# Optimization experiments

Hardware: AMD Instinct MI355X
Metric: run time of the kernel (lower is better)

## Reference

```python
import jax, jax.numpy as jnp
import numpy as np

N_ROI = 400
N_GRAPHS = 256
N = N_ROI * N_GRAPHS        # 102400 total nodes (stacked graphs)
E = N * 32                  # 3276800 edges, avg degree 32
T = 64                      # n_timepoints (in_channels of conv1)
H = 32                      # hidden channels of conv1/conv2
BS = 16                     # batch_size init arg = out_channels of conv3
N_CLASSES = 9


def setup_inputs() -> dict:
    key = jax.random.key(0)
    ks = jax.random.split(key, 20)
    s = 0.05
    p = {
        "x": jax.random.normal(ks[0], (N, T), jnp.float32),
        "edge_index": jax.random.randint(ks[1], (2, E), 0, N, dtype=jnp.int32),
        "edge_weight": jax.random.uniform(ks[2], (E,), jnp.float32),
        # ChebConv K=2: two bias-free linears + shared bias per layer
        "W1_0": jax.random.normal(ks[3], (T, H), jnp.float32) * s,
        "W1_1": jax.random.normal(ks[4], (T, H), jnp.float32) * s,
        "b1": jnp.zeros((H,), jnp.float32),
        "W2_0": jax.random.normal(ks[5], (H, H), jnp.float32) * s,
        "W2_1": jax.random.normal(ks[6], (H, H), jnp.float32) * s,
        "b2": jnp.zeros((H,), jnp.float32),
        "W3_0": jax.random.normal(ks[7], (H, BS), jnp.float32) * s,
        "W3_1": jax.random.normal(ks[8], (H, BS), jnp.float32) * s,
        "b3": jnp.zeros((BS,), jnp.float32),
        "fc1_w": jax.random.normal(ks[9], (N_ROI * BS, 256), jnp.float32) * s,
        "fc1_b": jnp.zeros((256,), jnp.float32),
        "fc2_w": jax.random.normal(ks[10], (256, 128), jnp.float32) * s,
        "fc2_b": jnp.zeros((128,), jnp.float32),
        "fc3_w": jax.random.normal(ks[11], (128, N_CLASSES), jnp.float32) * s,
        "fc3_b": jnp.zeros((N_CLASSES,), jnp.float32),
    }
    return p


def reference(x, edge_index, edge_weight, W1_0, W1_1, b1, W2_0, W2_1, b2,
              W3_0, W3_1, b3, fc1_w, fc1_b, fc2_w, fc2_b, fc3_w, fc3_b):
    src, dst = edge_index[0], edge_index[1]
    n = x.shape[0]
    # sym-normalized scaled Laplacian (lambda_max=2): Lhat = -D^-1/2 A D^-1/2
    deg = jax.ops.segment_sum(edge_weight, src, num_segments=n)
    deg_safe = jnp.where(deg > 0, deg, 1.0)
    dinv = jnp.where(deg > 0, jax.lax.rsqrt(deg_safe), 0.0)
    lapw = -(dinv[src] * edge_weight * dinv[dst])  # [E]

    def cheb(h, W0, W1, b):
        # K=2: Tx0 = h, Tx1 = Lhat @ h (gather-scatter over edges)
        tx1 = jax.ops.segment_sum(lapw[:, None] * h[src], dst, num_segments=n)
        return h @ W0 + tx1 @ W1 + b

    h = jax.nn.relu(cheb(x, W1_0, W1_1, b1))     # [N, 32]
    h = jax.nn.relu(cheb(h, W2_0, W2_1, b2))     # [N, 32]
    h = jax.nn.relu(cheb(h, W3_0, W3_1, b3))     # [N, 16]
    # global_mean_pool with batch=arange(N) is identity; reshape to graphs
    h = h.reshape(-1, N_ROI * BS)                # [256, 6400]
    h = h @ fc1_w + fc1_b                        # dropout is eval-mode identity
    h = h @ fc2_w + fc2_b
    return h @ fc3_w + fc3_b                     # [256, 9]
```

## Files before the change

### kernel.cpp

```cpp
#include <hip/hip_runtime.h>

#define NN   102400
#define NE   3276800
#define TT   64
#define HH   32
#define BSC  16
#define NG   256
#define NC   9
#define F1   256
#define F2   128
#define FIN  6400

#define NBUCK 200
#define CAP   18432
#define TILE  8192


__global__ __launch_bounds__(256) void k_init(int* __restrict__ scur,
                                              int* __restrict__ dcur) {
    int t = threadIdx.x;
    if (t < NBUCK) { scur[t] = t * CAP; dcur[t] = t * CAP; }
}

template<int MODE>
__global__ __launch_bounds__(256) void k_part(const int* __restrict__ src,
                                              const int* __restrict__ dst,
                                              const float* __restrict__ ew,
                                              int* __restrict__ gcur,
                                              int2* __restrict__ outbuf) {
    __shared__ int hist[256];
    __shared__ int base[256];
    __shared__ int cur[256];
    __shared__ int gpos[256];
    __shared__ int2 stage[TILE];
    __shared__ unsigned char bkt[TILE];

    int t = threadIdx.x;
    int e0 = blockIdx.x * TILE;

    hist[t] = 0;
    __syncthreads();
#pragma unroll
    for (int i = 0; i < TILE / 256; ++i) {
        int e = e0 + i * 256 + t;
        int key = MODE ? dst[e] : src[e];
        atomicAdd(&hist[key >> 9], 1);
    }
    __syncthreads();
    int h = hist[t];
    base[t] = h;
    __syncthreads();
    for (int off = 1; off < 256; off <<= 1) {
        int add = (t >= off) ? base[t - off] : 0;
        __syncthreads();
        base[t] += add;
        __syncthreads();
    }
    int excl = base[t] - h;
    __syncthreads();
    base[t] = excl;
    cur[t] = excl;
    __syncthreads();
#pragma unroll
    for (int i = 0; i < TILE / 256; ++i) {
        int e = e0 + i * 256 + t;
        int s = src[e];
        int w = __float_as_int(ew[e]);
        int key, pack;
        if (MODE) { int d = dst[e]; key = d; pack = (s << 9) | (d & 511); }
        else      { key = s; pack = s & 511; }
        int b = key >> 9;
        int p = atomicAdd(&cur[b], 1);
        stage[p] = make_int2(pack, w);
        bkt[p] = (unsigned char)b;
    }
    __syncthreads();
    if (t < NBUCK && h > 0) gpos[t] = atomicAdd(&gcur[t], h);
    __syncthreads();
#pragma unroll
    for (int i = 0; i < TILE / 256; ++i) {
        int p = i * 256 + t;
        int b = bkt[p];
        outbuf[gpos[b] + (p - base[b])] = stage[p];
    }
}


__global__ __launch_bounds__(512) void k_deg2(const int* __restrict__ scur,
                                              const int2* __restrict__ sbuck,
                                              float* __restrict__ dinv) {
    __shared__ float acc[512];
    int b = blockIdx.x, t = threadIdx.x;
    acc[t] = 0.f;
    __syncthreads();
    int lo = b * CAP, hi = scur[b];
    for (int j = lo + t; j < hi; j += 512) {
        int2 e = sbuck[j];
        atomicAdd(&acc[e.x], __int_as_float(e.y));
    }
    __syncthreads();
    float v = acc[t];
    dinv[b * 512 + t] = v > 0.f ? rsqrtf(v) : 0.f;
}


__global__ __launch_bounds__(512) void k_fin(const int* __restrict__ dcur,
                                             const int2* __restrict__ dbuck,
                                             const float* __restrict__ dinv,
                                             int2* __restrict__ edata,
                                             int* __restrict__ rowbeg,
                                             int* __restrict__ rowend) {
    __shared__ float dl[512];
    __shared__ int cnt[512];
    __shared__ int base[512];
    __shared__ int cur[512];
    int b = blockIdx.x, t = threadIdx.x;
    dl[t] = dinv[b * 512 + t];
    cnt[t] = 0;
    __syncthreads();
    int lo = b * CAP, hi = dcur[b];
    for (int j = lo + t; j < hi; j += 512)
        atomicAdd(&cnt[dbuck[j].x & 511], 1);
    __syncthreads();
    int h = cnt[t];
    base[t] = h;
    __syncthreads();
    for (int off = 1; off < 512; off <<= 1) {
        int add = (t >= off) ? base[t - off] : 0;
        __syncthreads();
        base[t] += add;
        __syncthreads();
    }
    int beg = lo + base[t] - h;
    rowbeg[b * 512 + t] = beg;
    rowend[b * 512 + t] = beg + h;
    cur[t] = beg;
    __syncthreads();
    for (int j = lo + t; j < hi; j += 512) {
        int2 e = dbuck[j];
        int dlow = e.x & 511;
        int s = e.x >> 9;
        float lw = -dinv[s] * __int_as_float(e.y) * dl[dlow];
        int slot = atomicAdd(&cur[dlow], 1);
        edata[slot] = make_int2(s, __float_as_int(lw));
    }
}


__global__ __launch_bounds__(256) void k_sortrows(const int* __restrict__ rowbeg,
                                                  const int* __restrict__ rowend,
                                                  int2* __restrict__ edata) {
    int wave = threadIdx.x >> 6;
    int lane = threadIdx.x & 63;
    int node = blockIdx.x * 4 + wave;
    int beg = rowbeg[node], end = rowend[node];
    int len = end - beg;
    if (len > 64 || len <= 1) return;
    unsigned long long key;
    if (lane < len) {
        int2 e = edata[beg + lane];
        key = ((unsigned long long)(unsigned)e.x << 32) | (unsigned)e.y;
    } else {
        key = ~0ULL;
    }
#pragma unroll
    for (int k = 2; k <= 64; k <<= 1) {
#pragma unroll
        for (int j = k >> 1; j >= 1; j >>= 1) {
            unsigned long long other = __shfl_xor(key, j, 64);
            bool lower = (lane & j) == 0;
            bool asc   = (lane & k) == 0;
            unsigned long long mn = key < other ? key : other;
            unsigned long long mx = key < other ? other : key;
            key = (lower == asc) ? mn : mx;
        }
    }
    if (lane < len) {
        edata[beg + lane] = make_int2((int)(key >> 32),
                                      (int)(unsigned)(key & 0xFFFFFFFFu));
    }
}

template<int CIN, int COUT>
__global__ __launch_bounds__(256) void k_dual_gemm(const float* __restrict__ in,
                                                   const float* __restrict__ W0,
                                                   const float* __restrict__ W1,
                                                   float* __restrict__ o0,
                                                   float* __restrict__ o1) {
    int node = blockIdx.x * 256 + threadIdx.x;
    const float* row = in + (size_t)node * CIN;
    float a0[COUT], a1[COUT];
#pragma unroll
    for (int c = 0; c < COUT; ++c) { a0[c] = 0.f; a1[c] = 0.f; }
    for (int k = 0; k < CIN; ++k) {
        float xv = row[k];
#pragma unroll
        for (int c = 0; c < COUT; ++c) {
            a0[c] = fmaf(xv, W0[k * COUT + c], a0[c]);
            a1[c] = fmaf(xv, W1[k * COUT + c], a1[c]);
        }
    }
#pragma unroll
    for (int c = 0; c < COUT; ++c) {
        o0[(size_t)node * COUT + c] = a0[c];
        o1[(size_t)node * COUT + c] = a1[c];
    }
}

template<int C>
__global__ __launch_bounds__(256) void k_gather(const int* __restrict__ rowbeg,
                                                const int* __restrict__ rowend,
                                                const int2* __restrict__ edata,
                                                const float* __restrict__ xw,
                                                const float* __restrict__ a,
                                                const float* __restrict__ bias,
                                                float* __restrict__ out) {
    constexpr int L = C / 2;
    constexpr int NPB = 256 / L;
    int tid = threadIdx.x;
    int g = tid / L;
    int lane = tid % L;
    int node = blockIdx.x * NPB + g;
    int start = rowbeg[node], end = rowend[node];
    const float2* xw2 = (const float2*)xw;
    float accx = 0.f, accy = 0.f;
    int j = start;
    for (; j + 7 < end; j += 8) {
        int2 e[8];
        float2 v[8];
#pragma unroll
        for (int u = 0; u < 8; ++u) e[u] = edata[j + u];
#pragma unroll
        for (int u = 0; u < 8; ++u) v[u] = xw2[(size_t)e[u].x * L + lane];
#pragma unroll
        for (int u = 0; u < 8; ++u) {
            float w = __int_as_float(e[u].y);
            accx = fmaf(w, v[u].x, accx);
            accy = fmaf(w, v[u].y, accy);
        }
    }
    for (; j < end; ++j) {
        int2 e0 = edata[j];
        float2 v0 = xw2[(size_t)e0.x * L + lane];
        float w = __int_as_float(e0.y);
        accx = fmaf(w, v0.x, accx);
        accy = fmaf(w, v0.y, accy);
    }
    float2 av = ((const float2*)a)[(size_t)node * L + lane];
    float2 bv = ((const float2*)bias)[lane];
    float rx = av.x + accx + bv.x;
    float ry = av.y + accy + bv.y;
    float2 r;
    r.x = rx > 0.f ? rx : 0.f;
    r.y = ry > 0.f ? ry : 0.f;
    ((float2*)out)[(size_t)node * L + lane] = r;
}

__global__ __launch_bounds__(256) void k_w23(const float* __restrict__ fc2w,
                                             const float* __restrict__ fc3w,
                                             float* __restrict__ w23) {
    int gid = blockIdx.x * 256 + threadIdx.x;
    if (gid >= F1 * NC) return;
    int r = gid / NC, c = gid % NC;
    float acc = 0.f;
    for (int j = 0; j < F2; ++j) acc = fmaf(fc2w[r * F2 + j], fc3w[j * NC + c], acc);
    w23[gid] = acc;
}

__global__ __launch_bounds__(64) void k_bc(const float* __restrict__ fc1b,
                                           const float* __restrict__ fc2b,
                                           const float* __restrict__ fc3b,
                                           const float* __restrict__ fc3w,
                                           const float* __restrict__ w23,
                                           float* __restrict__ bc) {
    int c = threadIdx.x;
    if (c >= NC) return;
    float acc = fc3b[c];
    for (int k = 0; k < F1; ++k) acc = fmaf(fc1b[k], w23[k * NC + c], acc);
    for (int j = 0; j < F2; ++j) acc = fmaf(fc2b[j], fc3w[j * NC + c], acc);
    bc[c] = acc;
}

__global__ __launch_bounds__(256) void k_t1(const float* __restrict__ fc1w,
                                            const float* __restrict__ fc2w,
                                            float* __restrict__ t1) {
    int c = threadIdx.x & 127;
    int rh = threadIdx.x >> 7;
    int r0 = blockIdx.x * 16 + rh;
    float acc[8];
#pragma unroll
    for (int rr = 0; rr < 8; ++rr) acc[rr] = 0.f;
    for (int k = 0; k < F1; ++k) {
        float wv = fc2w[k * F2 + c];
#pragma unroll
        for (int rr = 0; rr < 8; ++rr)
            acc[rr] = fmaf(fc1w[(r0 + rr * 2) * F1 + k], wv, acc[rr]);
    }
#pragma unroll
    for (int rr = 0; rr < 8; ++rr) t1[(r0 + rr * 2) * F2 + c] = acc[rr];
}

__global__ __launch_bounds__(256) void k_wc(const float* __restrict__ t1,
                                            const float* __restrict__ fc3w,
                                            float* __restrict__ wc) {
    int gid = blockIdx.x * 256 + threadIdx.x;
    int r = gid >> 4, c = gid & 15;
    if (c >= NC) return;
    float acc = 0.f;
    for (int j = 0; j < F2; ++j) acc = fmaf(t1[r * F2 + j], fc3w[j * NC + c], acc);
    wc[r * NC + c] = acc;
}

__global__ __launch_bounds__(256) void k_out(const float* __restrict__ h3,
                                             const float* __restrict__ wc,
                                             const float* __restrict__ bc,
                                             float* __restrict__ out) {
    __shared__ float red[256 * 10];
    int g = blockIdx.x, tid = threadIdx.x;
    float acc[NC];
#pragma unroll
    for (int c = 0; c < NC; ++c) acc[c] = 0.f;
    for (int k = tid; k < FIN; k += 256) {
        float hv = h3[(size_t)g * FIN + k];
#pragma unroll
        for (int c = 0; c < NC; ++c) acc[c] = fmaf(hv, wc[k * NC + c], acc[c]);
    }
#pragma unroll
    for (int c = 0; c < NC; ++c) red[tid * 10 + c] = acc[c];
    __syncthreads();
    for (int s = 128; s > 0; s >>= 1) {
        if (tid < s) {
#pragma unroll
            for (int c = 0; c < NC; ++c) red[tid * 10 + c] += red[(tid + s) * 10 + c];
        }
        __syncthreads();
    }
    if (tid < NC) out[g * NC + tid] = red[tid] + bc[tid];
}


extern "C" void kernel_launch(void* const* d_in, const int* in_sizes, int n_in,
                              void* d_out, int out_size, void* d_ws, size_t ws_size,
                              hipStream_t stream) {
    const float* x    = (const float*)d_in[0];
    const int*   ei   = (const int*)d_in[1];
    const float* ew   = (const float*)d_in[2];
    const float* W1_0 = (const float*)d_in[3];
    const float* W1_1 = (const float*)d_in[4];
    const float* b1   = (const float*)d_in[5];
    const float* W2_0 = (const float*)d_in[6];
    const float* W2_1 = (const float*)d_in[7];
    const float* b2   = (const float*)d_in[8];
    const float* W3_0 = (const float*)d_in[9];
    const float* W3_1 = (const float*)d_in[10];
    const float* b3   = (const float*)d_in[11];
    const float* fc1w = (const float*)d_in[12];
    const float* fc1b = (const float*)d_in[13];
    const float* fc2w = (const float*)d_in[14];
    const float* fc2b = (const float*)d_in[15];
    const float* fc3w = (const float*)d_in[16];
    const float* fc3b = (const float*)d_in[17];
    float* out = (float*)d_out;
    float* ws  = (float*)d_ws;

    const int* src = ei;
    const int* dst = ei + NE;

    const size_t REG = (size_t)NBUCK * CAP;
    float* dinv  = ws;
    int2*  dbuck = (int2*)(dinv + NN);
    int2*  sbuck = dbuck + REG;
    int2*  edata = sbuck;
    float* D     = (float*)(sbuck + REG);
    int*   rowbeg = (int*)(D + (size_t)NN * HH);
    int*   rowend = rowbeg + NN;
    int*   scur   = rowend + NN;
    int*   dcur   = scur + ((NBUCK + 1) & ~1);
    float* w23    = (float*)(dcur + ((NBUCK + 1) & ~1));
    float* bc     = w23 + F1 * NC;

    float* A = (float*)dbuck;
    float* B = A + (size_t)NN * HH;

    k_init<<<1, 256, 0, stream>>>(scur, dcur);
    k_part<0><<<NE / TILE, 256, 0, stream>>>(src, dst, ew, scur, sbuck);
    k_part<1><<<NE / TILE, 256, 0, stream>>>(src, dst, ew, dcur, dbuck);
    k_deg2<<<NBUCK, 512, 0, stream>>>(scur, sbuck, dinv);
    k_fin<<<NBUCK, 512, 0, stream>>>(dcur, dbuck, dinv, edata, rowbeg, rowend);
    k_sortrows<<<NN / 4, 256, 0, stream>>>(rowbeg, rowend, edata);

    k_dual_gemm<TT, HH><<<NN / 256, 256, 0, stream>>>(x, W1_0, W1_1, A, B);
    k_gather<HH><<<NN / 16, 256, 0, stream>>>(rowbeg, rowend, edata, B, A, b1, D);

    k_dual_gemm<HH, HH><<<NN / 256, 256, 0, stream>>>(D, W2_0, W2_1, A, B);
    k_gather<HH><<<NN / 16, 256, 0, stream>>>(rowbeg, rowend, edata, B, A, b2, D);

    k_dual_gemm<HH, BSC><<<NN / 256, 256, 0, stream>>>(D, W3_0, W3_1, A, B);
    k_gather<BSC><<<NN / 32, 256, 0, stream>>>(rowbeg, rowend, edata, B, A, b3, D);

    k_w23<<<(F1 * NC + 255) / 256, 256, 0, stream>>>(fc2w, fc3w, w23);
    k_bc<<<1, 64, 0, stream>>>(fc1b, fc2b, fc3b, fc3w, w23, bc);
    float* T1 = A;
    k_t1<<<FIN / 16, 256, 0, stream>>>(fc1w, fc2w, T1);
    float* Wc = B;
    k_wc<<<FIN * 16 / 256, 256, 0, stream>>>(T1, fc3w, Wc);
    k_out<<<NG, 256, 0, stream>>>(D, Wc, bc, out);
}
```

Measured before the change: 632.5 us.

## Fuse layer-2 gather with layer-3 dual GEMM and drop per-row edge sort

Removes the bitonic per-row sort of edge data and fuses the second Chebyshev gather with the third layer's dual linear transform via intra-group shuffles. This avoids writing and re-reading a 32-channel intermediate, one kernel launch, and the sort pass. Buffers are remapped so the later layer and head outputs fit in the freed regions. Unsorted rows make summation order nondeterministic and may reduce gather locality.

```diff
diff --git a/kernel.cpp b/kernel.cpp
--- a/kernel.cpp
+++ b/kernel.cpp
@@ -143,41 +143,6 @@
         float lw = -dinv[s] * __int_as_float(e.y) * dl[dlow];
         int slot = atomicAdd(&cur[dlow], 1);
         edata[slot] = make_int2(s, __float_as_int(lw));
-    }
-}
-
-
-__global__ __launch_bounds__(256) void k_sortrows(const int* __restrict__ rowbeg,
-                                                  const int* __restrict__ rowend,
-                                                  int2* __restrict__ edata) {
-    int wave = threadIdx.x >> 6;
-    int lane = threadIdx.x & 63;
-    int node = blockIdx.x * 4 + wave;
-    int beg = rowbeg[node], end = rowend[node];
-    int len = end - beg;
-    if (len > 64 || len <= 1) return;
-    unsigned long long key;
-    if (lane < len) {
-        int2 e = edata[beg + lane];
-        key = ((unsigned long long)(unsigned)e.x << 32) | (unsigned)e.y;
-    } else {
-        key = ~0ULL;
-    }
-#pragma unroll
-    for (int k = 2; k <= 64; k <<= 1) {
-#pragma unroll
-        for (int j = k >> 1; j >= 1; j >>= 1) {
-            unsigned long long other = __shfl_xor(key, j, 64);
-            bool lower = (lane & j) == 0;
-            bool asc   = (lane & k) == 0;
-            unsigned long long mn = key < other ? key : other;
-            unsigned long long mx = key < other ? other : key;
-            key = (lower == asc) ? mn : mx;
-        }
-    }
-    if (lane < len) {
-        edata[beg + lane] = make_int2((int)(key >> 32),
-                                      (int)(unsigned)(key & 0xFFFFFFFFu));
     }
 }
 
@@ -254,6 +219,63 @@
     r.x = rx > 0.f ? rx : 0.f;
     r.y = ry > 0.f ? ry : 0.f;
     ((float2*)out)[(size_t)node * L + lane] = r;
+}
+
+__global__ __launch_bounds__(256) void k_gather_gemm32(
+        const int* __restrict__ rowbeg, const int* __restrict__ rowend,
+        const int2* __restrict__ edata,
+        const float* __restrict__ xw, const float* __restrict__ a,
+        const float* __restrict__ bias,
+        const float* __restrict__ W0, const float* __restrict__ W1,
+        float* __restrict__ outA, float* __restrict__ outB) {
+    constexpr int L = 16;
+    constexpr int NPB = 256 / L;
+    int tid = threadIdx.x;
+    int g = tid / L;
+    int lane = tid % L;
+    int node = blockIdx.x * NPB + g;
+    int start = rowbeg[node], end = rowend[node];
+    const float2* xw2 = (const float2*)xw;
+    float accx = 0.f, accy = 0.f;
+    int j = start;
+    for (; j + 7 < end; j += 8) {
+        int2 e[8];
+        float2 v[8];
+#pragma unroll
+        for (int u = 0; u < 8; ++u) e[u] = edata[j + u];
+#pragma unroll
+        for (int u = 0; u < 8; ++u) v[u] = xw2[(size_t)e[u].x * L + lane];
+#pragma unroll
+        for (int u = 0; u < 8; ++u) {
+            float w = __int_as_float(e[u].y);
+            accx = fmaf(w, v[u].x, accx);
+            accy = fmaf(w, v[u].y, accy);
+        }
+    }
+    for (; j < end; ++j) {
+        int2 e0 = edata[j];
+        float2 v0 = xw2[(size_t)e0.x * L + lane];
+        float w = __int_as_float(e0.y);
+        accx = fmaf(w, v0.x, accx);
+        accy = fmaf(w, v0.y, accy);
+    }
+    float2 av = ((const float2*)a)[(size_t)node * L + lane];
+    float2 bv = ((const float2*)bias)[lane];
+    float h0 = av.x + accx + bv.x;  h0 = h0 > 0.f ? h0 : 0.f;
+    float h1 = av.y + accy + bv.y;  h1 = h1 > 0.f ? h1 : 0.f;
+    float a3 = 0.f, b3 = 0.f;
+#pragma unroll
+    for (int r = 0; r < 16; ++r) {
+        float hx = __shfl_xor(h0, r, 16);
+        float hy = __shfl_xor(h1, r, 16);
+        int m = lane ^ r;
+        a3 = fmaf(hx, W0[(2 * m) * 16 + lane], a3);
+        a3 = fmaf(hy, W0[(2 * m + 1) * 16 + lane], a3);
+        b3 = fmaf(hx, W1[(2 * m) * 16 + lane], b3);
+        b3 = fmaf(hy, W1[(2 * m + 1) * 16 + lane], b3);
+    }
+    outA[(size_t)node * 16 + lane] = a3;
+    outB[(size_t)node * 16 + lane] = b3;
 }
 
 __global__ __launch_bounds__(256) void k_w23(const float* __restrict__ fc2w,
@@ -371,8 +393,8 @@
     int2*  dbuck = (int2*)(dinv + NN);
     int2*  sbuck = dbuck + REG;
     int2*  edata = sbuck;
-    float* D     = (float*)(sbuck + REG);
-    int*   rowbeg = (int*)(D + (size_t)NN * HH);
+    float* Dreg  = (float*)(sbuck + REG);
+    int*   rowbeg = (int*)(Dreg + (size_t)NN * HH);
     int*   rowend = rowbeg + NN;
     int*   scur   = rowend + NN;
     int*   dcur   = scur + ((NBUCK + 1) & ~1);
@@ -381,28 +403,29 @@
 
     float* A = (float*)dbuck;
     float* B = A + (size_t)NN * HH;
+    float* A3 = Dreg;
+    float* B3 = Dreg + (size_t)NN * BSC;
+    float* h3 = (float*)dbuck;
+    float* T1 = (float*)dbuck + 2000000;
+    float* Wc = (float*)dbuck + 3000000;
 
     k_init<<<1, 256, 0, stream>>>(scur, dcur);
     k_part<0><<<NE / TILE, 256, 0, stream>>>(src, dst, ew, scur, sbuck);
     k_part<1><<<NE / TILE, 256, 0, stream>>>(src, dst, ew, dcur, dbuck);
     k_deg2<<<NBUCK, 512, 0, stream>>>(scur, sbuck, dinv);
     k_fin<<<NBUCK, 512, 0, stream>>>(dcur, dbuck, dinv, edata, rowbeg, rowend);
-    k_sortrows<<<NN / 4, 256, 0, stream>>>(rowbeg, rowend, edata);
 
     k_dual_gemm<TT, HH><<<NN / 256, 256, 0, stream>>>(x, W1_0, W1_1, A, B);
-    k_gather<HH><<<NN / 16, 256, 0, stream>>>(rowbeg, rowend, edata, B, A, b1, D);
-
-    k_dual_gemm<HH, HH><<<NN / 256, 256, 0, stream>>>(D, W2_0, W2_1, A, B);
-    k_gather<HH><<<NN / 16, 256, 0, stream>>>(rowbeg, rowend, edata, B, A, b2, D);
-
-    k_dual_gemm<HH, BSC><<<NN / 256, 256, 0, stream>>>(D, W3_0, W3_1, A, B);
-    k_gather<BSC><<<NN / 32, 256, 0, stream>>>(rowbeg, rowend, edata, B, A, b3, D);
+    k_gather<HH><<<NN / 16, 256, 0, stream>>>(rowbeg, rowend, edata, B, A, b1, Dreg);
+
+    k_dual_gemm<HH, HH><<<NN / 256, 256, 0, stream>>>(Dreg, W2_0, W2_1, A, B);
+    k_gather_gemm32<<<NN / 16, 256, 0, stream>>>(rowbeg, rowend, edata, B, A, b2,
+                                                 W3_0, W3_1, A3, B3);
+    k_gather<BSC><<<NN / 32, 256, 0, stream>>>(rowbeg, rowend, edata, B3, A3, b3, h3);
 
     k_w23<<<(F1 * NC + 255) / 256, 256, 0, stream>>>(fc2w, fc3w, w23);
     k_bc<<<1, 64, 0, stream>>>(fc1b, fc2b, fc3b, fc3w, w23, bc);
-    float* T1 = A;
     k_t1<<<FIN / 16, 256, 0, stream>>>(fc1w, fc2w, T1);
-    float* Wc = B;
     k_wc<<<FIN * 16 / 256, 256, 0, stream>>>(T1, fc3w, Wc);
-    k_out<<<NG, 256, 0, stream>>>(D, Wc, bc, out);
-}
+    k_out<<<NG, 256, 0, stream>>>(h3, Wc, bc, out);
+}
```

Measured after the change: 632.7 us. No clear change (+0.0%).
